# Performance work log

Measured on AMD Instinct MI355X. Metric: run time of the kernel, lower is better.

The kernel has to match this reference:

```python
import jax, jax.numpy as jnp
import numpy as np
import math

ALPHA_MIN = math.exp(-1.0 / 5.0)   # ~0.8187
ALPHA_MAX = math.exp(-1.0 / 25.0)  # ~0.9608
THRESHOLD = 1.0


def setup_inputs() -> dict:
    key = jax.random.key(0)
    k1, k2, k3, k4, k5 = jax.random.split(key, 5)
    B, T, I, H = 32, 2048, 256, 512
    x = jax.random.normal(k1, (B, T, I), dtype=jnp.float32)
    # Linear weight, kaiming-ish scale
    W = jax.random.normal(k2, (H, I), dtype=jnp.float32) * (1.0 / np.sqrt(I))
    # alpha ~ U[exp(-1/5), exp(-1/25)] as in nn.init.uniform_
    alpha = ALPHA_MIN + jax.random.uniform(k3, (H,), dtype=jnp.float32) * (ALPHA_MAX - ALPHA_MIN)
    # initial membrane potential / spike state (torch.rand in _lif_cell)
    u0 = jax.random.uniform(k4, (B, H), dtype=jnp.float32)
    s0 = jax.random.uniform(k5, (B, H), dtype=jnp.float32)
    return {"x": x, "W": W, "alpha": alpha, "u0": u0, "s0": s0}


def reference(x, W, alpha, u0, s0):
    # clamp alpha to its admissible range (lif_feature has no 'NoClamp')
    alpha = jnp.clip(alpha, ALPHA_MIN, ALPHA_MAX)
    b = 1.0 - alpha  # lif_feature has no 'B'

    # feedforward projection: [B, T, H]
    Wx = jnp.einsum('bti,hi->bth', x, W)

    def step(carry, wx_t):
        ut, st = carry
        ut = alpha * (ut - st) + b * wx_t          # leaky integrate + soft reset
        st = (ut - THRESHOLD > 0).astype(ut.dtype)  # heaviside spike
        return (ut, st), st

    # scan over time: Wx -> [T, B, H]
    _, s = jax.lax.scan(step, (u0, s0), jnp.swapaxes(Wx, 0, 1))
    return jnp.swapaxes(s, 0, 1)  # [B, T, H]
```

## Files before the change

### kernel.cpp

```cpp
#include <hip/hip_runtime.h>

#define ALPHA_MIN 0.8187307530779818f
#define ALPHA_MAX 0.9607894391523232f

typedef _Float16 f16;
typedef _Float16 f16x4 __attribute__((ext_vector_type(4)));
typedef _Float16 f16x8 __attribute__((ext_vector_type(8)));
typedef float f32x16 __attribute__((ext_vector_type(16)));

#define BB_ 32
#define TT_ 2048
#define KK_ 256
#define HH_ 512
#define TC_ 64
#define NC_ 32
#define KH_ 128

__device__ __forceinline__ void barrier_lds() {
    __builtin_amdgcn_s_waitcnt(0xC07F);
    __builtin_amdgcn_s_barrier();
}

__global__ __launch_bounds__(576, 1) void lif_fused7(
    const float* __restrict__ X,
    const float* __restrict__ W,
    const float* __restrict__ alpha,
    const float* __restrict__ u0,
    const float* __restrict__ s0,
    float* __restrict__ out)
{
    __shared__ f16 Ah[2][TC_ * KH_];
    __shared__ f16 Al[2][TC_ * KH_];
    __shared__ float wxbuf[2][TC_ * 64];

    const int b  = blockIdx.x & 31;
    const int nt = blockIdx.x >> 5;
    const int n0 = nt * 64;

    const int tid  = threadIdx.x;
    const int wv   = tid >> 6;
    const int lane = tid & 63;
    const int fm   = lane & 31;
    const int fq   = lane >> 5;

    if (wv < 4) {
        const int mh = wv >> 1;
        const int nh = wv & 1;

        f16x8 bh[16], bl[16];
        {
            const float* wp = W + (size_t)(n0 + nh * 32 + fm) * KK_ + fq * 8;
#pragma unroll
            for (int ks = 0; ks < 16; ++ks) {
                float4 v0 = *(const float4*)(wp + ks * 16);
                float4 v1 = *(const float4*)(wp + ks * 16 + 4);
                float v[8] = {v0.x, v0.y, v0.z, v0.w, v1.x, v1.y, v1.z, v1.w};
                f16x8 h, l;
#pragma unroll
                for (int j = 0; j < 8; ++j) {
                    const f16 hj = (f16)v[j];
                    h[j] = hj;
                    l[j] = (f16)((v[j] - (float)hj) * 2048.0f);
                }
                bh[ks] = h; bl[ks] = l;
            }
        }

        f32x16 accH, accLa, accLb;
#pragma unroll
        for (int e = 0; e < 16; ++e) { accH[e] = 0.0f; accLa[e] = 0.0f; accLb[e] = 0.0f; }

        const int row = mh * 32 + fm;
        const int r15 = row & 15;

        auto compute_half = [&](int hf) {
            __builtin_amdgcn_s_setprio(1);
#pragma unroll
            for (int ks = 0; ks < 8; ++ks) {
                const int addr = row * KH_ + (((ks * 2 + fq) ^ r15) * 8);
                const f16x8 ah = *(const f16x8*)&Ah[hf][addr];
                const f16x8 al = *(const f16x8*)&Al[hf][addr];
                const int ksg = hf * 8 + ks;
                accH  = __builtin_amdgcn_mfma_f32_32x32x16_f16(ah, bh[ksg], accH,  0, 0, 0);
                accLa = __builtin_amdgcn_mfma_f32_32x32x16_f16(ah, bl[ksg], accLa, 0, 0, 0);
                accLb = __builtin_amdgcn_mfma_f32_32x32x16_f16(al, bh[ksg], accLb, 0, 0, 0);
            }
            __builtin_amdgcn_s_setprio(0);
        };

        barrier_lds();
        for (int c = 0; c < NC_; ++c) {
            compute_half(0);
            barrier_lds();
            compute_half(1);
            {
                float* wb = &wxbuf[c & 1][0];
                const int colw = nh * 32 + fm;
#pragma unroll
                for (int r = 0; r < 16; ++r) {
                    const int roww = mh * 32 + (r & 3) + 8 * (r >> 2) + 4 * fq;
                    wb[roww * 64 + colw] = accH[r] + (accLa[r] + accLb[r]) * (1.0f / 2048.0f);
                    accH[r] = 0.0f; accLa[r] = 0.0f; accLb[r] = 0.0f;
                }
            }
            barrier_lds();
        }
    } else if (wv < 8) {
        const int u      = wv - 4;
        const int srow_j = u * 16 + (lane >> 5);
        const int f4i    = lane & 31;
        const int g      = f4i >> 1;
        const int sub    = f4i & 1;

        float4 pA[8], pB[8];

        auto issueA = [&](int hs) {
            const int c = hs >> 1, kh = hs & 1;
            const float* base = X + ((size_t)b * TT_ + c * TC_) * KK_ + kh * KH_ + f4i * 4;
#pragma unroll
            for (int j = 0; j < 8; ++j)
                pA[j] = *(const float4*)(base + (size_t)(srow_j + j * 2) * KK_);
        };
        auto issueB = [&](int hs) {
            const int c = hs >> 1, kh = hs & 1;
            const float* base = X + ((size_t)b * TT_ + c * TC_) * KK_ + kh * KH_ + f4i * 4;
#pragma unroll
            for (int j = 0; j < 8; ++j)
                pB[j] = *(const float4*)(base + (size_t)(srow_j + j * 2) * KK_);
        };
        auto cvtA = [&](int bufi) {
#pragma unroll
            for (int j = 0; j < 8; ++j) {
                const int rowa = srow_j + j * 2;
                const float v[4] = {pA[j].x, pA[j].y, pA[j].z, pA[j].w};
                f16x4 h, l;
#pragma unroll
                for (int e = 0; e < 4; ++e) {
                    const f16 he = (f16)v[e];
                    h[e] = he;
                    l[e] = (f16)((v[e] - (float)he) * 2048.0f);
                }
                const int addr = rowa * KH_ + ((g ^ (rowa & 15)) * 8) + sub * 4;
                *(f16x4*)&Ah[bufi][addr] = h;
                *(f16x4*)&Al[bufi][addr] = l;
            }
        };
        auto cvtB = [&](int bufi) {
#pragma unroll
            for (int j = 0; j < 8; ++j) {
                const int rowa = srow_j + j * 2;
                const float v[4] = {pB[j].x, pB[j].y, pB[j].z, pB[j].w};
                f16x4 h, l;
#pragma unroll
                for (int e = 0; e < 4; ++e) {
                    const f16 he = (f16)v[e];
                    h[e] = he;
                    l[e] = (f16)((v[e] - (float)he) * 2048.0f);
                }
                const int addr = rowa * KH_ + ((g ^ (rowa & 15)) * 8) + sub * 4;
                *(f16x4*)&Ah[bufi][addr] = h;
                *(f16x4*)&Al[bufi][addr] = l;
            }
        };

        issueA(0);
        issueB(1);
        cvtA(0);
        issueA(2);
        barrier_lds();

        for (int c = 0; c < NC_; ++c) {
            cvtB(1);
            if (c < NC_ - 1) issueB(2 * c + 3);
            barrier_lds();
            if (c < NC_ - 1) cvtA(0);
            if (c < NC_ - 2) issueA(2 * c + 4);
            barrier_lds();
        }
    } else {
        const int h = n0 + lane;
        const int chain = b * HH_ + h;
        float a = alpha[h];
        a = fminf(fmaxf(a, ALPHA_MIN), ALPHA_MAX);
        const float bbv = 1.0f - a;
        float u = u0[chain];
        float s = s0[chain];
        float* op = out + (size_t)b * TT_ * HH_ + h;

        auto consume = [&](int c, int hf) {
            const float* wb = &wxbuf[c & 1][0];
            const int tb = c * TC_ + hf * 32;
#pragma unroll
            for (int t0 = 0; t0 < 32; t0 += 8) {
                float w[8];
#pragma unroll
                for (int j = 0; j < 8; ++j) w[j] = wb[(hf * 32 + t0 + j) * 64 + lane];
#pragma unroll
                for (int j = 0; j < 8; ++j) {
                    u = fmaf(a, u - s, bbv * w[j]);
                    s = (u > 1.0f) ? 1.0f : 0.0f;
                    op[(size_t)(tb + t0 + j) * HH_] = s;
                }
            }
        };

        barrier_lds();
        for (int c = 0; c < NC_; ++c) {
            if (c) consume(c - 1, 0);
            barrier_lds();
            if (c) consume(c - 1, 1);
            barrier_lds();
        }
        consume(NC_ - 1, 0);
        consume(NC_ - 1, 1);
    }
}

__global__ void gemm_naive(const float* __restrict__ X, const float* __restrict__ W,
                           float* __restrict__ C, int M, int N, int K)
{
    const int idx = blockIdx.x * 256 + threadIdx.x;
    if (idx >= M * N) return;
    const int m = idx / N, n = idx % N;
    float acc = 0.0f;
    for (int k = 0; k < K; ++k) acc = fmaf(X[(size_t)m * K + k], W[(size_t)n * K + k], acc);
    C[idx] = acc;
}

__global__ __launch_bounds__(64) void lif_scan_inplace(
    float* __restrict__ buf, const float* __restrict__ alpha,
    const float* __restrict__ u0, const float* __restrict__ s0, int T, int H)
{
    const int chain = blockIdx.x * 64 + threadIdx.x;
    const int h = chain % H;
    const int b = chain / H;
    float a = alpha[h];
    a = fminf(fmaxf(a, ALPHA_MIN), ALPHA_MAX);
    const float bb = 1.0f - a;
    float u = u0[chain], s = s0[chain];
    float* base = buf + (size_t)b * T * H + h;
    for (int t = 0; t < T; ++t) {
        u = fmaf(a, u - s, bb * base[(size_t)t * H]);
        s = (u > 1.0f) ? 1.0f : 0.0f;
        base[(size_t)t * H] = s;
    }
}

extern "C" void kernel_launch(void* const* d_in, const int* in_sizes, int n_in,
                              void* d_out, int out_size, void* d_ws, size_t ws_size,
                              hipStream_t stream) {
    const float* x     = (const float*)d_in[0];
    const float* W     = (const float*)d_in[1];
    const float* alpha = (const float*)d_in[2];
    const float* u0    = (const float*)d_in[3];
    const float* s0    = (const float*)d_in[4];
    float* out = (float*)d_out;

    const int H = in_sizes[2];
    const int I = in_sizes[1] / H;
    const int B = in_sizes[3] / H;
    const int T = in_sizes[0] / (B * I);

    if (B == BB_ && T == TT_ && I == KK_ && H == HH_) {
        lif_fused7<<<256, 576, 0, stream>>>(x, W, alpha, u0, s0, out);
    } else {
        const int M = B * T;
        gemm_naive<<<(M * H + 255) / 256, 256, 0, stream>>>(x, W, out, M, H, I);
        lif_scan_inplace<<<(B * H + 63) / 64, 64, 0, stream>>>(out, alpha, u0, s0, T, H);
    }
}
```

Measured before the change: 275.6 us.

## Split fused GEMM+scan into separate time-split GEMM and register-pipelined scan kernels

Replaces the single fused kernel, where a scan wave consumed GEMM tiles from LDS, with two kernels. A GEMM kernel now splits time into two halves, giving 512 blocks, and writes Wx to global memory. A separate scan kernel then runs over 256 blocks of 64 threads and double-buffers 32-step loads in registers. This aims to raise GEMM parallelism and take the serial scan off the GEMM's critical path, at the cost of a full Wx round-trip through global memory and low occupancy in the scan kernel.

```diff
diff --git a/kernel.cpp b/kernel.cpp
--- a/kernel.cpp
+++ b/kernel.cpp
@@ -13,29 +13,28 @@
 #define KK_ 256
 #define HH_ 512
 #define TC_ 64
-#define NC_ 32
 #define KH_ 128
+#define CPB_ 16
 
 __device__ __forceinline__ void barrier_lds() {
     __builtin_amdgcn_s_waitcnt(0xC07F);
     __builtin_amdgcn_s_barrier();
 }
 
-__global__ __launch_bounds__(576, 1) void lif_fused7(
+__global__ __launch_bounds__(512, 1) void wx_gemm(
     const float* __restrict__ X,
     const float* __restrict__ W,
-    const float* __restrict__ alpha,
-    const float* __restrict__ u0,
-    const float* __restrict__ s0,
     float* __restrict__ out)
 {
     __shared__ f16 Ah[2][TC_ * KH_];
     __shared__ f16 Al[2][TC_ * KH_];
-    __shared__ float wxbuf[2][TC_ * 64];
-
-    const int b  = blockIdx.x & 31;
-    const int nt = blockIdx.x >> 5;
-    const int n0 = nt * 64;
+
+    const int b    = blockIdx.x & 31;
+    const int nt   = (blockIdx.x >> 5) & 7;
+    const int half = blockIdx.x >> 8;
+    const int n0   = nt * 64;
+    const int c0   = half * CPB_;
+    const int c1   = c0 + CPB_;
 
     const int tid  = threadIdx.x;
     const int wv   = tid >> 6;
@@ -89,23 +88,24 @@
         };
 
         barrier_lds();
-        for (int c = 0; c < NC_; ++c) {
+        for (int c = c0; c < c1; ++c) {
             compute_half(0);
             barrier_lds();
             compute_half(1);
             {
-                float* wb = &wxbuf[c & 1][0];
+                float* op = out + ((size_t)b * TT_ + (size_t)c * TC_) * HH_ + n0;
                 const int colw = nh * 32 + fm;
 #pragma unroll
                 for (int r = 0; r < 16; ++r) {
                     const int roww = mh * 32 + (r & 3) + 8 * (r >> 2) + 4 * fq;
-                    wb[roww * 64 + colw] = accH[r] + (accLa[r] + accLb[r]) * (1.0f / 2048.0f);
+                    op[(size_t)roww * HH_ + colw] =
+                        accH[r] + (accLa[r] + accLb[r]) * (1.0f / 2048.0f);
                     accH[r] = 0.0f; accLa[r] = 0.0f; accLb[r] = 0.0f;
                 }
             }
             barrier_lds();
         }
-    } else if (wv < 8) {
+    } else {
         const int u      = wv - 4;
         const int srow_j = u * 16 + (lane >> 5);
         const int f4i    = lane & 31;
@@ -116,14 +116,14 @@
 
         auto issueA = [&](int hs) {
             const int c = hs >> 1, kh = hs & 1;
-            const float* base = X + ((size_t)b * TT_ + c * TC_) * KK_ + kh * KH_ + f4i * 4;
+            const float* base = X + ((size_t)b * TT_ + (size_t)c * TC_) * KK_ + kh * KH_ + f4i * 4;
 #pragma unroll
             for (int j = 0; j < 8; ++j)
                 pA[j] = *(const float4*)(base + (size_t)(srow_j + j * 2) * KK_);
         };
         auto issueB = [&](int hs) {
             const int c = hs >> 1, kh = hs & 1;
-            const float* base = X + ((size_t)b * TT_ + c * TC_) * KK_ + kh * KH_ + f4i * 4;
+            const float* base = X + ((size_t)b * TT_ + (size_t)c * TC_) * KK_ + kh * KH_ + f4i * 4;
 #pragma unroll
             for (int j = 0; j < 8; ++j)
                 pB[j] = *(const float4*)(base + (size_t)(srow_j + j * 2) * KK_);
@@ -163,56 +163,72 @@
             }
         };
 
-        issueA(0);
-        issueB(1);
+        issueA(2 * c0);
+        issueB(2 * c0 + 1);
         cvtA(0);
-        issueA(2);
+        issueA(2 * c0 + 2);
         barrier_lds();
 
-        for (int c = 0; c < NC_; ++c) {
+        for (int c = c0; c < c1; ++c) {
             cvtB(1);
-            if (c < NC_ - 1) issueB(2 * c + 3);
-            barrier_lds();
-            if (c < NC_ - 1) cvtA(0);
-            if (c < NC_ - 2) issueA(2 * c + 4);
-            barrier_lds();
-        }
-    } else {
-        const int h = n0 + lane;
-        const int chain = b * HH_ + h;
-        float a = alpha[h];
-        a = fminf(fmaxf(a, ALPHA_MIN), ALPHA_MAX);
-        const float bbv = 1.0f - a;
-        float u = u0[chain];
-        float s = s0[chain];
-        float* op = out + (size_t)b * TT_ * HH_ + h;
-
-        auto consume = [&](int c, int hf) {
-            const float* wb = &wxbuf[c & 1][0];
-            const int tb = c * TC_ + hf * 32;
-#pragma unroll
-            for (int t0 = 0; t0 < 32; t0 += 8) {
-                float w[8];
-#pragma unroll
-                for (int j = 0; j < 8; ++j) w[j] = wb[(hf * 32 + t0 + j) * 64 + lane];
-#pragma unroll
-                for (int j = 0; j < 8; ++j) {
-                    u = fmaf(a, u - s, bbv * w[j]);
-                    s = (u > 1.0f) ? 1.0f : 0.0f;
-                    op[(size_t)(tb + t0 + j) * HH_] = s;
-                }
-            }
-        };
-
-        barrier_lds();
-        for (int c = 0; c < NC_; ++c) {
-            if (c) consume(c - 1, 0);
-            barrier_lds();
-            if (c) consume(c - 1, 1);
-            barrier_lds();
-        }
-        consume(NC_ - 1, 0);
-        consume(NC_ - 1, 1);
+            if (c + 1 < c1) issueB(2 * c + 3);
+            barrier_lds();
+            if (c + 1 < c1) cvtA(0);
+            if (c + 2 < c1) issueA(2 * c + 4);
+            barrier_lds();
+        }
+    }
+}
+
+__global__ __launch_bounds__(64) void lif_scan_opt(
+    float* __restrict__ buf,
+    const float* __restrict__ alpha,
+    const float* __restrict__ u0,
+    const float* __restrict__ s0)
+{
+    const int chain = blockIdx.x * 64 + threadIdx.x;
+    const int h = chain & (HH_ - 1);
+    const int b = chain >> 9;
+    float a = alpha[h];
+    a = fminf(fmaxf(a, ALPHA_MIN), ALPHA_MAX);
+    const float bbv = 1.0f - a;
+    float u = u0[chain];
+    float s = s0[chain];
+    float* base = buf + (size_t)b * TT_ * HH_ + h;
+
+    float wA[32], wB[32];
+
+    auto loadA = [&](int t0) {
+#pragma unroll
+        for (int i = 0; i < 32; ++i) wA[i] = base[(size_t)(t0 + i) * HH_];
+    };
+    auto loadB = [&](int t0) {
+#pragma unroll
+        for (int i = 0; i < 32; ++i) wB[i] = base[(size_t)(t0 + i) * HH_];
+    };
+    auto stepA = [&](int t0) {
+#pragma unroll
+        for (int i = 0; i < 32; ++i) {
+            u = fmaf(a, u - s, bbv * wA[i]);
+            s = (u > 1.0f) ? 1.0f : 0.0f;
+            base[(size_t)(t0 + i) * HH_] = s;
+        }
+    };
+    auto stepB = [&](int t0) {
+#pragma unroll
+        for (int i = 0; i < 32; ++i) {
+            u = fmaf(a, u - s, bbv * wB[i]);
+            s = (u > 1.0f) ? 1.0f : 0.0f;
+            base[(size_t)(t0 + i) * HH_] = s;
+        }
+    };
+
+    loadA(0);
+    for (int t0 = 0; t0 < TT_; t0 += 64) {
+        loadB(t0 + 32);
+        stepA(t0);
+        if (t0 + 64 < TT_) loadA(t0 + 64);
+        stepB(t0 + 32);
     }
 }
 
@@ -262,7 +278,8 @@
     const int T = in_sizes[0] / (B * I);
 
     if (B == BB_ && T == TT_ && I == KK_ && H == HH_) {
-        lif_fused7<<<256, 576, 0, stream>>>(x, W, alpha, u0, s0, out);
+        wx_gemm<<<512, 512, 0, stream>>>(x, W, out);
+        lif_scan_opt<<<256, 64, 0, stream>>>(out, alpha, u0, s0);
     } else {
         const int M = B * T;
         gemm_naive<<<(M * H + 255) / 256, 256, 0, stream>>>(x, W, out, M, H, I);
```

New measurement: 301.6 us. 9.4% more time.

## Split work into 32-column blocks to double block count and occupancy

Applied to the files above, without the earlier changes.

Each block now covers 32 hidden columns instead of 64, so there are 512 blocks of 7 waves (2 MFMA, 4 loader, 1 scan) in place of 256 blocks of 9 waves. The scan wave runs with only half its lanes writing output. The aim is more blocks across the CUs and more blocks per CU, so the serial time scan and X streaming overlap better. The cost is that each X tile is loaded and converted twice as often, doubling global reads of X, and the scan wave leaves half its lanes idle.

```diff
diff --git a/kernel.cpp b/kernel.cpp
--- a/kernel.cpp
+++ b/kernel.cpp
@@ -21,7 +21,7 @@
     __builtin_amdgcn_s_barrier();
 }
 
-__global__ __launch_bounds__(576, 1) void lif_fused7(
+__global__ __launch_bounds__(448, 4) void lif_fused8(
     const float* __restrict__ X,
     const float* __restrict__ W,
     const float* __restrict__ alpha,
@@ -31,11 +31,11 @@
 {
     __shared__ f16 Ah[2][TC_ * KH_];
     __shared__ f16 Al[2][TC_ * KH_];
-    __shared__ float wxbuf[2][TC_ * 64];
-
-    const int b  = blockIdx.x & 31;
-    const int nt = blockIdx.x >> 5;
-    const int n0 = nt * 64;
+    __shared__ float wxbuf[2][TC_ * 32];
+
+    const int b   = blockIdx.x & 31;
+    const int np  = blockIdx.x >> 5;
+    const int h0p = np * 32;
 
     const int tid  = threadIdx.x;
     const int wv   = tid >> 6;
@@ -43,13 +43,12 @@
     const int fm   = lane & 31;
     const int fq   = lane >> 5;
 
-    if (wv < 4) {
-        const int mh = wv >> 1;
-        const int nh = wv & 1;
+    if (wv < 2) {
+        const int mh = wv;
 
         f16x8 bh[16], bl[16];
         {
-            const float* wp = W + (size_t)(n0 + nh * 32 + fm) * KK_ + fq * 8;
+            const float* wp = W + (size_t)(h0p + fm) * KK_ + fq * 8;
 #pragma unroll
             for (int ks = 0; ks < 16; ++ks) {
                 float4 v0 = *(const float4*)(wp + ks * 16);
@@ -95,18 +94,17 @@
             compute_half(1);
             {
                 float* wb = &wxbuf[c & 1][0];
-                const int colw = nh * 32 + fm;
 #pragma unroll
                 for (int r = 0; r < 16; ++r) {
                     const int roww = mh * 32 + (r & 3) + 8 * (r >> 2) + 4 * fq;
-                    wb[roww * 64 + colw] = accH[r] + (accLa[r] + accLb[r]) * (1.0f / 2048.0f);
+                    wb[roww * 32 + fm] = accH[r] + (accLa[r] + accLb[r]) * (1.0f / 2048.0f);
                     accH[r] = 0.0f; accLa[r] = 0.0f; accLb[r] = 0.0f;
                 }
             }
             barrier_lds();
         }
-    } else if (wv < 8) {
-        const int u      = wv - 4;
+    } else if (wv < 6) {
+        const int u      = wv - 2;
         const int srow_j = u * 16 + (lane >> 5);
         const int f4i    = lane & 31;
         const int g      = f4i >> 1;
@@ -116,14 +114,14 @@
 
         auto issueA = [&](int hs) {
             const int c = hs >> 1, kh = hs & 1;
-            const float* base = X + ((size_t)b * TT_ + c * TC_) * KK_ + kh * KH_ + f4i * 4;
+            const float* base = X + ((size_t)b * TT_ + (size_t)c * TC_) * KK_ + kh * KH_ + f4i * 4;
 #pragma unroll
             for (int j = 0; j < 8; ++j)
                 pA[j] = *(const float4*)(base + (size_t)(srow_j + j * 2) * KK_);
         };
         auto issueB = [&](int hs) {
             const int c = hs >> 1, kh = hs & 1;
-            const float* base = X + ((size_t)b * TT_ + c * TC_) * KK_ + kh * KH_ + f4i * 4;
+            const float* base = X + ((size_t)b * TT_ + (size_t)c * TC_) * KK_ + kh * KH_ + f4i * 4;
 #pragma unroll
             for (int j = 0; j < 8; ++j)
                 pB[j] = *(const float4*)(base + (size_t)(srow_j + j * 2) * KK_);
@@ -171,15 +169,17 @@
 
         for (int c = 0; c < NC_; ++c) {
             cvtB(1);
-            if (c < NC_ - 1) issueB(2 * c + 3);
-            barrier_lds();
-            if (c < NC_ - 1) cvtA(0);
-            if (c < NC_ - 2) issueA(2 * c + 4);
+            if (c + 1 < NC_) issueB(2 * c + 3);
+            barrier_lds();
+            if (c + 1 < NC_) cvtA(0);
+            if (c + 2 < NC_) issueA(2 * c + 4);
             barrier_lds();
         }
     } else {
-        const int h = n0 + lane;
+        const int hx = lane & 31;
+        const int h  = h0p + hx;
         const int chain = b * HH_ + h;
+        const bool active = (lane < 32);
         float a = alpha[h];
         a = fminf(fmaxf(a, ALPHA_MIN), ALPHA_MAX);
         const float bbv = 1.0f - a;
@@ -194,12 +194,12 @@
             for (int t0 = 0; t0 < 32; t0 += 8) {
                 float w[8];
 #pragma unroll
-                for (int j = 0; j < 8; ++j) w[j] = wb[(hf * 32 + t0 + j) * 64 + lane];
+                for (int j = 0; j < 8; ++j) w[j] = wb[(hf * 32 + t0 + j) * 32 + hx];
 #pragma unroll
                 for (int j = 0; j < 8; ++j) {
                     u = fmaf(a, u - s, bbv * w[j]);
                     s = (u > 1.0f) ? 1.0f : 0.0f;
-                    op[(size_t)(tb + t0 + j) * HH_] = s;
+                    if (active) op[(size_t)(tb + t0 + j) * HH_] = s;
                 }
             }
         };
@@ -262,7 +262,7 @@
     const int T = in_sizes[0] / (B * I);
 
     if (B == BB_ && T == TT_ && I == KK_ && H == HH_) {
-        lif_fused7<<<256, 576, 0, stream>>>(x, W, alpha, u0, s0, out);
+        lif_fused8<<<512, 448, 0, stream>>>(x, W, alpha, u0, s0, out);
     } else {
         const int M = B * T;
         gemm_naive<<<(M * H + 255) / 256, 256, 0, stream>>>(x, W, out, M, H, I);
```

Measured after the change: 346.6 us. +25.8%, slower.
